# Kernel tuning notes

Hardware: AMD Instinct MI355X
Metric: run time of the kernel (lower is better)

## Reference

```python
import jax, jax.numpy as jnp
import numpy as np

B, C_IN, C_OUT, H, W, K = 8, 64, 64, 128, 128, 3
KK = K * K


def _conv(x, w, b):
    # 3x3, stride 1, padding 1 (matches nn.Conv2d(stride=1, padding=1))
    y = jax.lax.conv_general_dilated(
        x, w, window_strides=(1, 1), padding=((1, 1), (1, 1)),
        dimension_numbers=('NCHW', 'OIHW', 'NCHW'))
    return y + b[None, :, None, None]


def setup_inputs() -> dict:
    key = jax.random.key(0)
    k1, k2, k3, k4, k5 = jax.random.split(key, 5)
    x = jax.random.normal(k1, (B, C_IN, H, W), jnp.float32)
    s = 1.0 / np.sqrt(C_IN * K * K)  # torch conv default init range
    w_off = jax.random.uniform(k2, (2 * KK, C_IN, K, K), jnp.float32, -s, s)
    b_off = jax.random.uniform(k3, (2 * KK,), jnp.float32, -s, s)
    w_reg = jax.random.uniform(k4, (C_OUT, C_IN, K, K), jnp.float32, -s, s)
    b_reg = jax.random.uniform(k5, (C_OUT,), jnp.float32, -s, s)
    return {"x": x, "w_off": w_off, "b_off": b_off, "w_reg": w_reg, "b_reg": b_reg}


def _deform_sample(x, offsets):
    # Equivalent of the K*K grid_sample(align_corners=True, padding_mode='zeros')
    # loop + sum over kernel positions. The norm/unnorm cancel, so sampling is
    # at absolute pixel coords base_grid + offsets.
    B_, C, H_, W_ = x.shape
    off = offsets.reshape(B_, KK, 2, H_, W_).transpose(0, 3, 4, 1, 2)  # B,H,W,KK,2
    xs = off[..., 0] + jnp.arange(W_, dtype=x.dtype)[None, None, :, None]
    ys = off[..., 1] + jnp.arange(H_, dtype=x.dtype)[None, :, None, None]
    x0 = jnp.floor(xs)
    y0 = jnp.floor(ys)
    wx1 = xs - x0
    wx0 = 1.0 - wx1
    wy1 = ys - y0
    wy0 = 1.0 - wy1
    x_flat = x.reshape(B_, C, H_ * W_)

    def gather(yi, xi, w):
        valid = (xi >= 0) & (xi < W_) & (yi >= 0) & (yi < H_)  # zeros padding
        xi_c = jnp.clip(xi, 0, W_ - 1).astype(jnp.int32)
        yi_c = jnp.clip(yi, 0, H_ - 1).astype(jnp.int32)
        idx = (yi_c * W_ + xi_c).reshape(B_, 1, H_ * W_ * KK)
        g = jnp.take_along_axis(
            x_flat, jnp.broadcast_to(idx, (B_, C, H_ * W_ * KK)), axis=2)
        g = g.reshape(B_, C, H_, W_, KK)
        wm = (w * valid.astype(x.dtype))[:, None]  # B,1,H,W,KK
        return (g * wm).sum(-1)  # sum over the KK kernel positions

    return (gather(y0, x0, wy0 * wx0)
            + gather(y0, x0 + 1.0, wy0 * wx1)
            + gather(y0 + 1.0, x0, wy1 * wx0)
            + gather(y0 + 1.0, x0 + 1.0, wy1 * wx1))


def reference(x, w_off, b_off, w_reg, b_reg):
    offsets = _conv(x, w_off, b_off)          # B, 2*KK, H, W
    sampled = _deform_sample(x, offsets)      # B, C, H, W (summed over KK)
    return _conv(sampled, w_reg, b_reg)       # B, C_OUT, H, W
```

## Files before the change

kernel.cpp:

```cpp
#include <hip/hip_runtime.h>

#define B_ 8
#define CIN 64
#define COUT 64
#define H_ 128
#define W_ 128
#define HW (H_*W_)
#define OFFP 24

typedef __attribute__((ext_vector_type(8))) short short8;
typedef __attribute__((ext_vector_type(4))) float f32x4;

__device__ __forceinline__ short f2bf(float f) {
    unsigned u = __float_as_uint(f);
    unsigned r = (u + 0x7fffu + ((u >> 16) & 1u)) >> 16;
    return (short)r;
}
__device__ __forceinline__ float bf2f(short s) {
    return __uint_as_float(((unsigned)(unsigned short)s) << 16);
}

template<int NT>
__device__ __forceinline__ void prep_one(const float* __restrict__ w, short* __restrict__ o,
                                         int i, int n_used) {
    int j = i & 7, lane = (i >> 3) & 63, rest = i >> 9;
    int nt = rest % NT, dc = rest / NT, c = dc & 1, d = dc >> 1;
    int oc = nt * 16 + (lane & 15);
    int ic = c * 32 + (lane >> 4) * 8 + j;
    float v = (oc < n_used) ? w[(oc * 64 + ic) * 9 + d] : 0.f;
    o[i] = f2bf(v);
}

__global__ __launch_bounds__(256) void k_tr(const float* __restrict__ x,
                                            short* __restrict__ xt,
                                            const float* __restrict__ wof,
                                            const float* __restrict__ wrg,
                                            short* __restrict__ wt1,
                                            short* __restrict__ wt2) {
    int i = blockIdx.x * 256 + threadIdx.x;
    if (i < 9 * 2 * 2 * 512) prep_one<2>(wof, wt1, i, 18);
    if (i < 9 * 2 * 4 * 512) prep_one<4>(wrg, wt2, i, 64);

    __shared__ float tile[64 * 129];
    int bh = blockIdx.x;
    int bb = bh & 7, h = bh >> 3;
    const float* xp = x + (size_t)bb * (CIN * HW) + h * W_;
#pragma unroll
    for (int j = 0; j < 32; ++j) {
        int e = threadIdx.x + 256 * j;
        int cc = e >> 7, ww = e & 127;
        tile[cc * 129 + ww] = __builtin_nontemporal_load(xp + cc * HW + ww);
    }
    __syncthreads();
    short* op = xt + (((size_t)(bb << 7) + h) << 13);
#pragma unroll
    for (int j = 0; j < 32; ++j) {
        int e = threadIdx.x + 256 * j;
        int ww = e >> 6, cc = e & 63;
        op[e] = f2bf(tile[cc * 129 + ww]);
    }
}

template<int NT, bool TO_OFF>
__global__ __launch_bounds__(1024, 4) void k_conv(const short* __restrict__ src,
                                                  const short* __restrict__ wt,
                                                  const float* __restrict__ bias,
                                                  short* __restrict__ outb,
                                                  float* __restrict__ outf) {
    __shared__ short At[6 * 130 * 64];
    int blk = blockIdx.x;
    int bb = blk & 7;
    int h0 = (blk >> 3) << 2;

#pragma unroll
    for (int it = 0; it < 7; ++it) {
        int s = threadIdx.x + it * 1024;
        if (s < 6240) {
            int r = s / 1040, rem = s % 1040;
            int px = rem >> 3, ck = rem & 7;
            int y = h0 - 1 + r, xx = px - 1;
            bool v = ((unsigned)y < H_) && ((unsigned)xx < W_);
            int yc = min(max(y, 0), H_ - 1), xc = min(max(xx, 0), W_ - 1);
            short8 val = *(const short8*)(src + ((((size_t)(bb << 7) + yc) << 7) + xc) * 64 + ck * 8);
            short8 z = {0,0,0,0,0,0,0,0};
            if (!v) val = z;
            *(short8*)(&At[(r * 130 + px) * 64 + ((ck ^ (px & 7)) << 3)]) = val;
        }
    }
    __syncthreads();

    int lane = threadIdx.x & 63;
    int wave = threadIdx.x >> 6;
    int lr = wave >> 2;
    int p0 = (wave & 3) * 32;
    int m = lane & 15, quad = lane >> 4;

    f32x4 acc[2][NT];
#pragma unroll
    for (int nt = 0; nt < NT; ++nt) {
        int oc = nt * 16 + m;
        float bv = (!TO_OFF || oc < 18) ? bias[oc] : 0.f;
#pragma unroll
        for (int mt = 0; mt < 2; ++mt) {
            acc[mt][nt][0] = bv; acc[mt][nt][1] = bv;
            acc[mt][nt][2] = bv; acc[mt][nt][3] = bv;
        }
    }

#pragma unroll
    for (int d = 0; d < 9; ++d) {
        int dy = d / 3, dx = d % 3;
#pragma unroll
        for (int c = 0; c < 2; ++c) {
            short8 a[2];
#pragma unroll
            for (int mt = 0; mt < 2; ++mt) {
                int px = p0 + mt * 16 + m + dx;
                a[mt] = *(const short8*)(&At[((lr + dy) * 130 + px) * 64 + (((c * 4 + quad) ^ (px & 7)) << 3)]);
            }
#pragma unroll
            for (int nt = 0; nt < NT; ++nt) {
                short8 b = *(const short8*)(wt + ((((d * 2 + c) * NT + nt) * 64 + lane) << 3));
#pragma unroll
                for (int mt = 0; mt < 2; ++mt)
                    acc[mt][nt] = __builtin_amdgcn_mfma_f32_16x16x32_bf16(a[mt], b, acc[mt][nt], 0, 0, 0);
            }
        }
    }

    if (TO_OFF) {
        __syncthreads();
        unsigned short* St = (unsigned short*)At;
#pragma unroll
        for (int nt = 0; nt < NT; ++nt) {
            int oc = nt * 16 + m;
            if (oc < 20) {
#pragma unroll
                for (int mt = 0; mt < 2; ++mt) {
                    int pl = lr * 128 + p0 + mt * 16 + quad * 4;
#pragma unroll
                    for (int r = 0; r < 4; ++r)
                        St[(pl + r) * OFFP + oc] = (unsigned short)f2bf(acc[mt][nt][r]);
                }
            }
        }
        __syncthreads();
        const unsigned* Sd = (const unsigned*)St;
        unsigned* Od = (unsigned*)(outb + ((size_t)((bb << 14) + (h0 << 7))) * OFFP);
#pragma unroll
        for (int j = 0; j < 6; ++j)
            Od[threadIdx.x + 1024 * j] = Sd[threadIdx.x + 1024 * j];
    } else {
#pragma unroll
        for (int nt = 0; nt < NT; ++nt) {
            int oc = nt * 16 + m;
#pragma unroll
            for (int mt = 0; mt < 2; ++mt) {
                int wpix = p0 + mt * 16 + quad * 4;
                __builtin_nontemporal_store(acc[mt][nt],
                    (f32x4*)(outf + (((size_t)(bb * 64 + oc)) << 14) + ((h0 + lr) << 7) + wpix));
            }
        }
    }
}

__device__ __forceinline__ void prep3(const unsigned* __restrict__ myo, int g,
                                      int w, int h, int cko,
                                      int* __restrict__ eo, float* __restrict__ wg) {
#pragma unroll
    for (int t = 0; t < 3; ++t) {
        unsigned owk = myo[g * 3 + t];
        float ox = bf2f((short)(owk & 0xffff));
        float oy = bf2f((short)(owk >> 16));
        float xs = (float)w + ox, ys = (float)h + oy;
        float x0f = floorf(xs), y0f = floorf(ys);
        float wx1 = xs - x0f, wx0 = 1.f - wx1;
        float wy1 = ys - y0f, wy0 = 1.f - wy1;
        int x0 = (int)x0f, y0 = (int)y0f;
        int x1 = x0 + 1, y1 = y0 + 1;
        int x0c = min(max(x0, 0), W_ - 1), x1c = min(max(x1, 0), W_ - 1);
        int y0c = min(max(y0, 0), H_ - 1), y1c = min(max(y1, 0), H_ - 1);
        bool vx0 = ((unsigned)x0 < W_), vx1 = ((unsigned)x1 < W_);
        bool vy0 = ((unsigned)y0 < H_), vy1 = ((unsigned)y1 < H_);
        wg[t * 4 + 0] = (vy0 && vx0) ? wy0 * wx0 : 0.f;
        wg[t * 4 + 1] = (vy0 && vx1) ? wy0 * wx1 : 0.f;
        wg[t * 4 + 2] = (vy1 && vx0) ? wy1 * wx0 : 0.f;
        wg[t * 4 + 3] = (vy1 && vx1) ? wy1 * wx1 : 0.f;
        eo[t * 4 + 0] = ((y0c * W_ + x0c) << 6) + cko;
        eo[t * 4 + 1] = ((y0c * W_ + x1c) << 6) + cko;
        eo[t * 4 + 2] = ((y1c * W_ + x0c) << 6) + cko;
        eo[t * 4 + 3] = ((y1c * W_ + x1c) << 6) + cko;
    }
}

__global__ __launch_bounds__(256, 2) void k_sample(const short* __restrict__ xt,
                                                   const short* __restrict__ offb,
                                                   short* __restrict__ smp) {
    __shared__ unsigned sow[4 * 96];
    int blk = blockIdx.x;
    int bb = blk & 7;
    int tile = blk >> 3;
    int tw = tile & 15, th = tile >> 4;

    {
        int rowid = threadIdx.x >> 6, rl = threadIdx.x & 63;
        const unsigned* srcp = (const unsigned*)(offb +
            ((size_t)((bb << 14) + (((th << 2) + rowid) << 7) + (tw << 3))) * OFFP);
        sow[rowid * 96 + rl] = __builtin_nontemporal_load(srcp + rl);
        if (rl < 32) sow[rowid * 96 + 64 + rl] = __builtin_nontemporal_load(srcp + 64 + rl);
    }
    __syncthreads();

    int lp = threadIdx.x >> 3;
    int ck = threadIdx.x & 7;
    int w = (tw << 3) + (lp & 7);
    int h = (th << 2) + (lp >> 3);
    int pix = (bb << 14) + (h << 7) + w;
    const short* xim = xt + ((size_t)bb << 20);
    int cko = ck * 8;
    const unsigned* myo = &sow[(lp >> 3) * 96 + (lp & 7) * 12];

    int eo[12];
    float wgtA[12], wgtB[12], wgtC[12];
    short8 vA[12], vB[12], vC[12];
    float acc[8];
#pragma unroll
    for (int i = 0; i < 8; ++i) acc[i] = 0.f;

    prep3(myo, 0, w, h, cko, eo, wgtA);
#pragma unroll
    for (int n = 0; n < 12; ++n) vA[n] = *(const short8*)(xim + eo[n]);
    prep3(myo, 1, w, h, cko, eo, wgtB);
#pragma unroll
    for (int n = 0; n < 12; ++n) vB[n] = *(const short8*)(xim + eo[n]);
    prep3(myo, 2, w, h, cko, eo, wgtC);
#pragma unroll
    for (int n = 0; n < 12; ++n) vC[n] = *(const short8*)(xim + eo[n]);

#pragma unroll
    for (int n = 0; n < 12; ++n) {
        float wv = wgtA[n];
#pragma unroll
        for (int i = 0; i < 8; ++i) acc[i] += wv * bf2f(vA[n][i]);
    }
#pragma unroll
    for (int n = 0; n < 12; ++n) {
        float wv = wgtB[n];
#pragma unroll
        for (int i = 0; i < 8; ++i) acc[i] += wv * bf2f(vB[n][i]);
    }
#pragma unroll
    for (int n = 0; n < 12; ++n) {
        float wv = wgtC[n];
#pragma unroll
        for (int i = 0; i < 8; ++i) acc[i] += wv * bf2f(vC[n][i]);
    }

    short8 o;
#pragma unroll
    for (int i = 0; i < 8; ++i) o[i] = f2bf(acc[i]);
    *(short8*)(smp + (size_t)pix * 64 + cko) = o;
}

extern "C" void kernel_launch(void* const* d_in, const int* in_sizes, int n_in,
                              void* d_out, int out_size, void* d_ws, size_t ws_size,
                              hipStream_t stream) {
    const float* x   = (const float*)d_in[0];
    const float* wof = (const float*)d_in[1];
    const float* bof = (const float*)d_in[2];
    const float* wrg = (const float*)d_in[3];
    const float* brg = (const float*)d_in[4];
    float* out = (float*)d_out;

    char* ws = (char*)d_ws;
    short* xt   = (short*)ws;
    short* smp  = (short*)(ws + 16777216);
    short* offb = (short*)(ws + 2 * 16777216);
    short* wt1  = (short*)(ws + 2 * 16777216 + 6291456);
    short* wt2  = (short*)(ws + 2 * 16777216 + 6291456 + 36864);

    k_tr   <<<dim3(B_ * H_), 256, 0, stream>>>(x, xt, wof, wrg, wt1, wt2);
    k_conv<2, true>  <<<dim3(B_ * H_ / 4), 1024, 0, stream>>>(xt, wt1, bof, offb, nullptr);
    k_sample<<<dim3((B_ * HW * 8) / 256), 256, 0, stream>>>(xt, offb, smp);
    k_conv<4, false> <<<dim3(B_ * H_ / 4), 1024, 0, stream>>>(smp, wt2, brg, nullptr, out);
}
```

Before: 148.5 us.

## Share bilinear tap preparation across channel lanes via LDS and vectorize transpose stores

```diff
diff --git a/kernel.cpp b/kernel.cpp
--- a/kernel.cpp
+++ b/kernel.cpp
@@ -54,10 +54,13 @@
     __syncthreads();
     short* op = xt + (((size_t)(bb << 7) + h) << 13);
 #pragma unroll
-    for (int j = 0; j < 32; ++j) {
-        int e = threadIdx.x + 256 * j;
-        int ww = e >> 6, cc = e & 63;
-        op[e] = f2bf(tile[cc * 129 + ww]);
+    for (int j = 0; j < 4; ++j) {
+        int t = threadIdx.x + 256 * j;
+        int ww = t >> 3, c0 = (t & 7) << 3;
+        short8 o;
+#pragma unroll
+        for (int k = 0; k < 8; ++k) o[k] = f2bf(tile[(c0 + k) * 129 + ww]);
+        *(short8*)(op + ww * 64 + c0) = o;
     }
 }
 
@@ -164,39 +167,42 @@
     }
 }
 
-__device__ __forceinline__ void prep3(const unsigned* __restrict__ myo, int g,
-                                      int w, int h, int cko,
-                                      int* __restrict__ eo, float* __restrict__ wg) {
-#pragma unroll
-    for (int t = 0; t < 3; ++t) {
-        unsigned owk = myo[g * 3 + t];
-        float ox = bf2f((short)(owk & 0xffff));
-        float oy = bf2f((short)(owk >> 16));
-        float xs = (float)w + ox, ys = (float)h + oy;
-        float x0f = floorf(xs), y0f = floorf(ys);
-        float wx1 = xs - x0f, wx0 = 1.f - wx1;
-        float wy1 = ys - y0f, wy0 = 1.f - wy1;
-        int x0 = (int)x0f, y0 = (int)y0f;
-        int x1 = x0 + 1, y1 = y0 + 1;
-        int x0c = min(max(x0, 0), W_ - 1), x1c = min(max(x1, 0), W_ - 1);
-        int y0c = min(max(y0, 0), H_ - 1), y1c = min(max(y1, 0), H_ - 1);
-        bool vx0 = ((unsigned)x0 < W_), vx1 = ((unsigned)x1 < W_);
-        bool vy0 = ((unsigned)y0 < H_), vy1 = ((unsigned)y1 < H_);
-        wg[t * 4 + 0] = (vy0 && vx0) ? wy0 * wx0 : 0.f;
-        wg[t * 4 + 1] = (vy0 && vx1) ? wy0 * wx1 : 0.f;
-        wg[t * 4 + 2] = (vy1 && vx0) ? wy1 * wx0 : 0.f;
-        wg[t * 4 + 3] = (vy1 && vx1) ? wy1 * wx1 : 0.f;
-        eo[t * 4 + 0] = ((y0c * W_ + x0c) << 6) + cko;
-        eo[t * 4 + 1] = ((y0c * W_ + x1c) << 6) + cko;
-        eo[t * 4 + 2] = ((y1c * W_ + x0c) << 6) + cko;
-        eo[t * 4 + 3] = ((y1c * W_ + x1c) << 6) + cko;
-    }
+__device__ __forceinline__ void prep_task(int task, int tw, int th,
+                                          const unsigned* __restrict__ sow,
+                                          int* __restrict__ seo,
+                                          float* __restrict__ swg) {
+    int px = task / 9, tap = task - px * 9;
+    unsigned owk = sow[(px >> 3) * 96 + (px & 7) * 12 + tap];
+    float ox = bf2f((short)(owk & 0xffff));
+    float oy = bf2f((short)(owk >> 16));
+    float xs = (float)((tw << 3) + (px & 7)) + ox;
+    float ys = (float)((th << 2) + (px >> 3)) + oy;
+    float x0f = floorf(xs), y0f = floorf(ys);
+    float wx1 = xs - x0f, wx0 = 1.f - wx1;
+    float wy1 = ys - y0f, wy0 = 1.f - wy1;
+    int x0 = (int)x0f, y0 = (int)y0f;
+    int x1 = x0 + 1, y1 = y0 + 1;
+    int x0c = min(max(x0, 0), W_ - 1), x1c = min(max(x1, 0), W_ - 1);
+    int y0c = min(max(y0, 0), H_ - 1), y1c = min(max(y1, 0), H_ - 1);
+    bool vx0 = ((unsigned)x0 < W_), vx1 = ((unsigned)x1 < W_);
+    bool vy0 = ((unsigned)y0 < H_), vy1 = ((unsigned)y1 < H_);
+    int bse = task << 2;
+    swg[bse + 0] = (vy0 && vx0) ? wy0 * wx0 : 0.f;
+    swg[bse + 1] = (vy0 && vx1) ? wy0 * wx1 : 0.f;
+    swg[bse + 2] = (vy1 && vx0) ? wy1 * wx0 : 0.f;
+    swg[bse + 3] = (vy1 && vx1) ? wy1 * wx1 : 0.f;
+    seo[bse + 0] = (y0c * W_ + x0c) << 6;
+    seo[bse + 1] = (y0c * W_ + x1c) << 6;
+    seo[bse + 2] = (y1c * W_ + x0c) << 6;
+    seo[bse + 3] = (y1c * W_ + x1c) << 6;
 }
 
 __global__ __launch_bounds__(256, 2) void k_sample(const short* __restrict__ xt,
                                                    const short* __restrict__ offb,
                                                    short* __restrict__ smp) {
     __shared__ unsigned sow[4 * 96];
+    __shared__ int   seo[288 * 4];
+    __shared__ float swg[288 * 4];
     int blk = blockIdx.x;
     int bb = blk & 7;
     int tile = blk >> 3;
@@ -211,49 +217,32 @@
     }
     __syncthreads();
 
+    prep_task(threadIdx.x, tw, th, sow, seo, swg);
+    if (threadIdx.x < 32) prep_task(threadIdx.x + 256, tw, th, sow, seo, swg);
+    __syncthreads();
+
     int lp = threadIdx.x >> 3;
     int ck = threadIdx.x & 7;
+    int cko = ck * 8;
     int w = (tw << 3) + (lp & 7);
     int h = (th << 2) + (lp >> 3);
     int pix = (bb << 14) + (h << 7) + w;
-    const short* xim = xt + ((size_t)bb << 20);
-    int cko = ck * 8;
-    const unsigned* myo = &sow[(lp >> 3) * 96 + (lp & 7) * 12];
-
-    int eo[12];
-    float wgtA[12], wgtB[12], wgtC[12];
-    short8 vA[12], vB[12], vC[12];
+    const short* xim = xt + ((size_t)bb << 20) + cko;
+    const int* __restrict__ meo = &seo[lp * 36];
+    const float* __restrict__ mwg = &swg[lp * 36];
+
+    short8 v[36];
+#pragma unroll
+    for (int n = 0; n < 36; ++n) v[n] = *(const short8*)(xim + meo[n]);
+
     float acc[8];
 #pragma unroll
     for (int i = 0; i < 8; ++i) acc[i] = 0.f;
-
-    prep3(myo, 0, w, h, cko, eo, wgtA);
-#pragma unroll
-    for (int n = 0; n < 12; ++n) vA[n] = *(const short8*)(xim + eo[n]);
-    prep3(myo, 1, w, h, cko, eo, wgtB);
-#pragma unroll
-    for (int n = 0; n < 12; ++n) vB[n] = *(const short8*)(xim + eo[n]);
-    prep3(myo, 2, w, h, cko, eo, wgtC);
-#pragma unroll
-    for (int n = 0; n < 12; ++n) vC[n] = *(const short8*)(xim + eo[n]);
-
-#pragma unroll
-    for (int n = 0; n < 12; ++n) {
-        float wv = wgtA[n];
-#pragma unroll
-        for (int i = 0; i < 8; ++i) acc[i] += wv * bf2f(vA[n][i]);
-    }
-#pragma unroll
-    for (int n = 0; n < 12; ++n) {
-        float wv = wgtB[n];
-#pragma unroll
-        for (int i = 0; i < 8; ++i) acc[i] += wv * bf2f(vB[n][i]);
-    }
-#pragma unroll
-    for (int n = 0; n < 12; ++n) {
-        float wv = wgtC[n];
-#pragma unroll
-        for (int i = 0; i < 8; ++i) acc[i] += wv * bf2f(vC[n][i]);
+#pragma unroll
+    for (int n = 0; n < 36; ++n) {
+        float wv = mwg[n];
+#pragma unroll
+        for (int i = 0; i < 8; ++i) acc[i] += wv * bf2f(v[n][i]);
     }
 
     short8 o;
```

After: 146.3 us. About the same (-1.5%).

## Fuse transpose, offset conv, sampling and regular conv into one cooperative kernel

Applied to the files above, without the earlier changes.

```diff
diff --git a/kernel.cpp b/kernel.cpp
--- a/kernel.cpp
+++ b/kernel.cpp
@@ -1,4 +1,7 @@
 #include <hip/hip_runtime.h>
+#include <hip/hip_cooperative_groups.h>
+
+namespace cg = cooperative_groups;
 
 #define B_ 8
 #define CIN 64
@@ -29,139 +32,6 @@
     int ic = c * 32 + (lane >> 4) * 8 + j;
     float v = (oc < n_used) ? w[(oc * 64 + ic) * 9 + d] : 0.f;
     o[i] = f2bf(v);
-}
-
-__global__ __launch_bounds__(256) void k_tr(const float* __restrict__ x,
-                                            short* __restrict__ xt,
-                                            const float* __restrict__ wof,
-                                            const float* __restrict__ wrg,
-                                            short* __restrict__ wt1,
-                                            short* __restrict__ wt2) {
-    int i = blockIdx.x * 256 + threadIdx.x;
-    if (i < 9 * 2 * 2 * 512) prep_one<2>(wof, wt1, i, 18);
-    if (i < 9 * 2 * 4 * 512) prep_one<4>(wrg, wt2, i, 64);
-
-    __shared__ float tile[64 * 129];
-    int bh = blockIdx.x;
-    int bb = bh & 7, h = bh >> 3;
-    const float* xp = x + (size_t)bb * (CIN * HW) + h * W_;
-#pragma unroll
-    for (int j = 0; j < 32; ++j) {
-        int e = threadIdx.x + 256 * j;
-        int cc = e >> 7, ww = e & 127;
-        tile[cc * 129 + ww] = __builtin_nontemporal_load(xp + cc * HW + ww);
-    }
-    __syncthreads();
-    short* op = xt + (((size_t)(bb << 7) + h) << 13);
-#pragma unroll
-    for (int j = 0; j < 32; ++j) {
-        int e = threadIdx.x + 256 * j;
-        int ww = e >> 6, cc = e & 63;
-        op[e] = f2bf(tile[cc * 129 + ww]);
-    }
-}
-
-template<int NT, bool TO_OFF>
-__global__ __launch_bounds__(1024, 4) void k_conv(const short* __restrict__ src,
-                                                  const short* __restrict__ wt,
-                                                  const float* __restrict__ bias,
-                                                  short* __restrict__ outb,
-                                                  float* __restrict__ outf) {
-    __shared__ short At[6 * 130 * 64];
-    int blk = blockIdx.x;
-    int bb = blk & 7;
-    int h0 = (blk >> 3) << 2;
-
-#pragma unroll
-    for (int it = 0; it < 7; ++it) {
-        int s = threadIdx.x + it * 1024;
-        if (s < 6240) {
-            int r = s / 1040, rem = s % 1040;
-            int px = rem >> 3, ck = rem & 7;
-            int y = h0 - 1 + r, xx = px - 1;
-            bool v = ((unsigned)y < H_) && ((unsigned)xx < W_);
-            int yc = min(max(y, 0), H_ - 1), xc = min(max(xx, 0), W_ - 1);
-            short8 val = *(const short8*)(src + ((((size_t)(bb << 7) + yc) << 7) + xc) * 64 + ck * 8);
-            short8 z = {0,0,0,0,0,0,0,0};
-            if (!v) val = z;
-            *(short8*)(&At[(r * 130 + px) * 64 + ((ck ^ (px & 7)) << 3)]) = val;
-        }
-    }
-    __syncthreads();
-
-    int lane = threadIdx.x & 63;
-    int wave = threadIdx.x >> 6;
-    int lr = wave >> 2;
-    int p0 = (wave & 3) * 32;
-    int m = lane & 15, quad = lane >> 4;
-
-    f32x4 acc[2][NT];
-#pragma unroll
-    for (int nt = 0; nt < NT; ++nt) {
-        int oc = nt * 16 + m;
-        float bv = (!TO_OFF || oc < 18) ? bias[oc] : 0.f;
-#pragma unroll
-        for (int mt = 0; mt < 2; ++mt) {
-            acc[mt][nt][0] = bv; acc[mt][nt][1] = bv;
-            acc[mt][nt][2] = bv; acc[mt][nt][3] = bv;
-        }
-    }
-
-#pragma unroll
-    for (int d = 0; d < 9; ++d) {
-        int dy = d / 3, dx = d % 3;
-#pragma unroll
-        for (int c = 0; c < 2; ++c) {
-            short8 a[2];
-#pragma unroll
-            for (int mt = 0; mt < 2; ++mt) {
-                int px = p0 + mt * 16 + m + dx;
-                a[mt] = *(const short8*)(&At[((lr + dy) * 130 + px) * 64 + (((c * 4 + quad) ^ (px & 7)) << 3)]);
-            }
-#pragma unroll
-            for (int nt = 0; nt < NT; ++nt) {
-                short8 b = *(const short8*)(wt + ((((d * 2 + c) * NT + nt) * 64 + lane) << 3));
-#pragma unroll
-                for (int mt = 0; mt < 2; ++mt)
-                    acc[mt][nt] = __builtin_amdgcn_mfma_f32_16x16x32_bf16(a[mt], b, acc[mt][nt], 0, 0, 0);
-            }
-        }
-    }
-
-    if (TO_OFF) {
-        __syncthreads();
-        unsigned short* St = (unsigned short*)At;
-#pragma unroll
-        for (int nt = 0; nt < NT; ++nt) {
-            int oc = nt * 16 + m;
-            if (oc < 20) {
-#pragma unroll
-                for (int mt = 0; mt < 2; ++mt) {
-                    int pl = lr * 128 + p0 + mt * 16 + quad * 4;
-#pragma unroll
-                    for (int r = 0; r < 4; ++r)
-                        St[(pl + r) * OFFP + oc] = (unsigned short)f2bf(acc[mt][nt][r]);
-                }
-            }
-        }
-        __syncthreads();
-        const unsigned* Sd = (const unsigned*)St;
-        unsigned* Od = (unsigned*)(outb + ((size_t)((bb << 14) + (h0 << 7))) * OFFP);
-#pragma unroll
-        for (int j = 0; j < 6; ++j)
-            Od[threadIdx.x + 1024 * j] = Sd[threadIdx.x + 1024 * j];
-    } else {
-#pragma unroll
-        for (int nt = 0; nt < NT; ++nt) {
-            int oc = nt * 16 + m;
-#pragma unroll
-            for (int mt = 0; mt < 2; ++mt) {
-                int wpix = p0 + mt * 16 + quad * 4;
-                __builtin_nontemporal_store(acc[mt][nt],
-                    (f32x4*)(outf + (((size_t)(bb * 64 + oc)) << 14) + ((h0 + lr) << 7) + wpix));
-            }
-        }
-    }
 }
 
 __device__ __forceinline__ void prep3(const unsigned* __restrict__ myo, int g,
@@ -193,73 +63,228 @@
     }
 }
 
-__global__ __launch_bounds__(256, 2) void k_sample(const short* __restrict__ xt,
-                                                   const short* __restrict__ offb,
-                                                   short* __restrict__ smp) {
-    __shared__ unsigned sow[4 * 96];
+__global__ __launch_bounds__(1024, 4) void k_fused(
+        const float* __restrict__ x,
+        short* __restrict__ xt,
+        const float* __restrict__ wof,
+        const float* __restrict__ wrg,
+        short* __restrict__ wt1,
+        short* __restrict__ wt2,
+        const float* __restrict__ bof,
+        const float* __restrict__ brg,
+        short* __restrict__ smp,
+        float* __restrict__ out) {
+    __shared__ short lds[62208];
+    short* S = lds;
+    unsigned short* St = (unsigned short*)(lds + 49920);
+
     int blk = blockIdx.x;
+    int tid = threadIdx.x;
+
+    {
+        int i = blk * 1024 + tid;
+        if (i < 9 * 2 * 2 * 512) prep_one<2>(wof, wt1, i, 18);
+        if (i < 9 * 2 * 4 * 512) prep_one<4>(wrg, wt2, i, 64);
+
+        float* tile = (float*)lds;
+        for (int q = 0; q < 4; ++q) {
+            int s = blk * 4 + q;
+            int bb0 = s & 7, h = s >> 3;
+            const float* xp = x + (size_t)bb0 * (CIN * HW) + h * W_;
+            __syncthreads();
+#pragma unroll
+            for (int j = 0; j < 8; ++j) {
+                int e = tid + 1024 * j;
+                int cc = e >> 7, ww = e & 127;
+                tile[cc * 129 + ww] = __builtin_nontemporal_load(xp + cc * HW + ww);
+            }
+            __syncthreads();
+            short* op = xt + (((size_t)(bb0 << 7) + h) << 13);
+            int ww = tid >> 3, c0 = (tid & 7) << 3;
+            short8 o;
+#pragma unroll
+            for (int k = 0; k < 8; ++k) o[k] = f2bf(tile[(c0 + k) * 129 + ww]);
+            *(short8*)(op + ww * 64 + c0) = o;
+        }
+    }
+
+    cg::this_grid().sync();
+
     int bb = blk & 7;
-    int tile = blk >> 3;
-    int tw = tile & 15, th = tile >> 4;
+    int h0 = (blk >> 3) << 2;
+    int lane = tid & 63;
+    int wave = tid >> 6;
+    int lr = wave >> 2;
+    int p0 = (wave & 3) * 32;
+    int m = lane & 15, quad = lane >> 4;
+
+#pragma unroll
+    for (int it = 0; it < 7; ++it) {
+        int s = tid + it * 1024;
+        if (s < 6240) {
+            int r = s / 1040, rem = s % 1040;
+            int px = rem >> 3, ck = rem & 7;
+            int y = h0 - 1 + r, xx = px - 1;
+            bool v = ((unsigned)y < H_) && ((unsigned)xx < W_);
+            int yc = min(max(y, 0), H_ - 1), xc = min(max(xx, 0), W_ - 1);
+            short8 val = *(const short8*)(xt + ((((size_t)(bb << 7) + yc) << 7) + xc) * 64 + ck * 8);
+            short8 z = {0, 0, 0, 0, 0, 0, 0, 0};
+            if (!v) val = z;
+            *(short8*)(&S[(r * 130 + px) * 64 + ((ck ^ (px & 7)) << 3)]) = val;
+        }
+    }
+    __syncthreads();
 
     {
-        int rowid = threadIdx.x >> 6, rl = threadIdx.x & 63;
-        const unsigned* srcp = (const unsigned*)(offb +
-            ((size_t)((bb << 14) + (((th << 2) + rowid) << 7) + (tw << 3))) * OFFP);
-        sow[rowid * 96 + rl] = __builtin_nontemporal_load(srcp + rl);
-        if (rl < 32) sow[rowid * 96 + 64 + rl] = __builtin_nontemporal_load(srcp + 64 + rl);
+        f32x4 acc[2][2];
+#pragma unroll
+        for (int nt = 0; nt < 2; ++nt) {
+            int oc = nt * 16 + m;
+            float bv = (oc < 18) ? bof[oc] : 0.f;
+#pragma unroll
+            for (int mt = 0; mt < 2; ++mt) {
+                acc[mt][nt][0] = bv; acc[mt][nt][1] = bv;
+                acc[mt][nt][2] = bv; acc[mt][nt][3] = bv;
+            }
+        }
+#pragma unroll
+        for (int d = 0; d < 9; ++d) {
+            int dy = d / 3, dx = d % 3;
+#pragma unroll
+            for (int c = 0; c < 2; ++c) {
+                short8 a[2];
+#pragma unroll
+                for (int mt = 0; mt < 2; ++mt) {
+                    int px = p0 + mt * 16 + m + dx;
+                    a[mt] = *(const short8*)(&S[((lr + dy) * 130 + px) * 64 + (((c * 4 + quad) ^ (px & 7)) << 3)]);
+                }
+#pragma unroll
+                for (int nt = 0; nt < 2; ++nt) {
+                    short8 b = *(const short8*)(wt1 + ((((d * 2 + c) * 2 + nt) * 64 + lane) << 3));
+#pragma unroll
+                    for (int mt = 0; mt < 2; ++mt)
+                        acc[mt][nt] = __builtin_amdgcn_mfma_f32_16x16x32_bf16(a[mt], b, acc[mt][nt], 0, 0, 0);
+                }
+            }
+        }
+#pragma unroll
+        for (int nt = 0; nt < 2; ++nt) {
+            int oc = nt * 16 + m;
+            if (oc < 18) {
+#pragma unroll
+                for (int mt = 0; mt < 2; ++mt) {
+                    int pl = lr * 128 + p0 + mt * 16 + quad * 4;
+#pragma unroll
+                    for (int r = 0; r < 4; ++r)
+                        St[(pl + r) * OFFP + oc] = (unsigned short)f2bf(acc[mt][nt][r]);
+                }
+            }
+        }
     }
     __syncthreads();
 
-    int lp = threadIdx.x >> 3;
-    int ck = threadIdx.x & 7;
-    int w = (tw << 3) + (lp & 7);
-    int h = (th << 2) + (lp >> 3);
-    int pix = (bb << 14) + (h << 7) + w;
-    const short* xim = xt + ((size_t)bb << 20);
-    int cko = ck * 8;
-    const unsigned* myo = &sow[(lp >> 3) * 96 + (lp & 7) * 12];
-
-    int eo[12];
-    float wgtA[12], wgtB[12], wgtC[12];
-    short8 vA[12], vB[12], vC[12];
-    float acc[8];
-#pragma unroll
-    for (int i = 0; i < 8; ++i) acc[i] = 0.f;
-
-    prep3(myo, 0, w, h, cko, eo, wgtA);
-#pragma unroll
-    for (int n = 0; n < 12; ++n) vA[n] = *(const short8*)(xim + eo[n]);
-    prep3(myo, 1, w, h, cko, eo, wgtB);
-#pragma unroll
-    for (int n = 0; n < 12; ++n) vB[n] = *(const short8*)(xim + eo[n]);
-    prep3(myo, 2, w, h, cko, eo, wgtC);
-#pragma unroll
-    for (int n = 0; n < 12; ++n) vC[n] = *(const short8*)(xim + eo[n]);
-
-#pragma unroll
-    for (int n = 0; n < 12; ++n) {
-        float wv = wgtA[n];
-#pragma unroll
-        for (int i = 0; i < 8; ++i) acc[i] += wv * bf2f(vA[n][i]);
-    }
-#pragma unroll
-    for (int n = 0; n < 12; ++n) {
-        float wv = wgtB[n];
-#pragma unroll
-        for (int i = 0; i < 8; ++i) acc[i] += wv * bf2f(vB[n][i]);
-    }
-#pragma unroll
-    for (int n = 0; n < 12; ++n) {
-        float wv = wgtC[n];
-#pragma unroll
-        for (int i = 0; i < 8; ++i) acc[i] += wv * bf2f(vC[n][i]);
-    }
-
-    short8 o;
-#pragma unroll
-    for (int i = 0; i < 8; ++i) o[i] = f2bf(acc[i]);
-    *(short8*)(smp + (size_t)pix * 64 + cko) = o;
+    {
+        int ck = tid & 7, sx = tid >> 3;
+        int cko = ck * 8;
+        const short* xim = xt + ((size_t)bb << 20);
+        for (int row = 0; row < 4; ++row) {
+            int y = h0 + row;
+            const unsigned* myo = (const unsigned*)(St + (row * 128 + sx) * OFFP);
+            float acc[8];
+#pragma unroll
+            for (int i = 0; i < 8; ++i) acc[i] = 0.f;
+#pragma unroll
+            for (int g = 0; g < 3; ++g) {
+                int eo[12]; float wg[12]; short8 v[12];
+                prep3(myo, g, sx, y, cko, eo, wg);
+#pragma unroll
+                for (int n = 0; n < 12; ++n) v[n] = *(const short8*)(xim + eo[n]);
+#pragma unroll
+                for (int n = 0; n < 12; ++n) {
+                    float wv = wg[n];
+#pragma unroll
+                    for (int i = 0; i < 8; ++i) acc[i] += wv * bf2f(v[n][i]);
+                }
+            }
+            short8 o;
+#pragma unroll
+            for (int i = 0; i < 8; ++i) o[i] = f2bf(acc[i]);
+            *(short8*)(&S[((row + 1) * 130 + (sx + 1)) * 64 + ((ck ^ ((sx + 1) & 7)) << 3)]) = o;
+            if (row == 0 || row == 3)
+                *(short8*)(smp + ((((size_t)(bb << 7) + y) << 7) + sx) * 64 + cko) = o;
+        }
+    }
+
+    cg::this_grid().sync();
+
+#pragma unroll
+    for (int it = 0; it < 3; ++it) {
+        int s = tid + it * 1024;
+        if (s < 2080) {
+            int rr = s / 1040, rem = s % 1040;
+            int px = rem >> 3, ck = rem & 7;
+            int r = rr * 5;
+            int y = h0 - 1 + r, xx = px - 1;
+            bool v = ((unsigned)y < H_) && ((unsigned)xx < W_);
+            int yc = min(max(y, 0), H_ - 1), xc = min(max(xx, 0), W_ - 1);
+            short8 val = *(const short8*)(smp + ((((size_t)(bb << 7) + yc) << 7) + xc) * 64 + ck * 8);
+            short8 z = {0, 0, 0, 0, 0, 0, 0, 0};
+            if (!v) val = z;
+            *(short8*)(&S[(r * 130 + px) * 64 + ((ck ^ (px & 7)) << 3)]) = val;
+        }
+    }
+    if (tid < 64) {
+        int r = 1 + (tid >> 4);
+        int px = ((tid >> 3) & 1) * 129;
+        int ck = tid & 7;
+        short8 z = {0, 0, 0, 0, 0, 0, 0, 0};
+        *(short8*)(&S[(r * 130 + px) * 64 + ((ck ^ (px & 7)) << 3)]) = z;
+    }
+    __syncthreads();
+
+    {
+        f32x4 acc[2][4];
+#pragma unroll
+        for (int nt = 0; nt < 4; ++nt) {
+            int oc = nt * 16 + m;
+            float bv = brg[oc];
+#pragma unroll
+            for (int mt = 0; mt < 2; ++mt) {
+                acc[mt][nt][0] = bv; acc[mt][nt][1] = bv;
+                acc[mt][nt][2] = bv; acc[mt][nt][3] = bv;
+            }
+        }
+#pragma unroll
+        for (int d = 0; d < 9; ++d) {
+            int dy = d / 3, dx = d % 3;
+#pragma unroll
+            for (int c = 0; c < 2; ++c) {
+                short8 a[2];
+#pragma unroll
+                for (int mt = 0; mt < 2; ++mt) {
+                    int px = p0 + mt * 16 + m + dx;
+                    a[mt] = *(const short8*)(&S[((lr + dy) * 130 + px) * 64 + (((c * 4 + quad) ^ (px & 7)) << 3)]);
+                }
+#pragma unroll
+                for (int nt = 0; nt < 4; ++nt) {
+                    short8 b = *(const short8*)(wt2 + ((((d * 2 + c) * 4 + nt) * 64 + lane) << 3));
+#pragma unroll
+                    for (int mt = 0; mt < 2; ++mt)
+                        acc[mt][nt] = __builtin_amdgcn_mfma_f32_16x16x32_bf16(a[mt], b, acc[mt][nt], 0, 0, 0);
+                }
+            }
+        }
+#pragma unroll
+        for (int nt = 0; nt < 4; ++nt) {
+            int oc = nt * 16 + m;
+#pragma unroll
+            for (int mt = 0; mt < 2; ++mt) {
+                int wpix = p0 + mt * 16 + quad * 4;
+                __builtin_nontemporal_store(acc[mt][nt],
+                    (f32x4*)(out + (((size_t)(bb * 64 + oc)) << 14) + ((h0 + lr) << 7) + wpix));
+            }
+        }
+    }
 }
 
 extern "C" void kernel_launch(void* const* d_in, const int* in_sizes, int n_in,
@@ -273,14 +298,14 @@
     float* out = (float*)d_out;
 
     char* ws = (char*)d_ws;
-    short* xt   = (short*)ws;
-    short* smp  = (short*)(ws + 16777216);
-    short* offb = (short*)(ws + 2 * 16777216);
-    short* wt1  = (short*)(ws + 2 * 16777216 + 6291456);
-    short* wt2  = (short*)(ws + 2 * 16777216 + 6291456 + 36864);
-
-    k_tr   <<<dim3(B_ * H_), 256, 0, stream>>>(x, xt, wof, wrg, wt1, wt2);
-    k_conv<2, true>  <<<dim3(B_ * H_ / 4), 1024, 0, stream>>>(xt, wt1, bof, offb, nullptr);
-    k_sample<<<dim3((B_ * HW * 8) / 256), 256, 0, stream>>>(xt, offb, smp);
-    k_conv<4, false> <<<dim3(B_ * H_ / 4), 1024, 0, stream>>>(smp, wt2, brg, nullptr, out);
-}
+    short* xt  = (short*)ws;
+    short* smp = (short*)(ws + 16777216);
+    short* wt1 = (short*)(ws + 2 * 16777216);
+    short* wt2 = (short*)(ws + 2 * 16777216 + 36864);
+
+    void* args[] = {(void*)&x, (void*)&xt, (void*)&wof, (void*)&wrg,
+                    (void*)&wt1, (void*)&wt2, (void*)&bof, (void*)&brg,
+                    (void*)&smp, (void*)&out};
+    hipLaunchCooperativeKernel((const void*)k_fused, dim3(256), dim3(1024),
+                               args, 0, stream);
+}
```

New measurement: 231.9 us. +56.2%, slower.
